# Kernel tuning notes

Hardware: AMD Instinct MI355X
Metric: run time of the kernel (lower is better)

The kernel has to match this reference:

```python
import jax, jax.numpy as jnp
import numpy as np

B, D_IN, UNITS, D_OUT = 16384, 1024, 512, 512
T_END = 0.1  # ODE integrated over t in (0, 0.1)


def setup_inputs() -> dict:
    key = jax.random.key(0)
    ks = jax.random.split(key, 8)
    return {
        "x": jax.random.normal(ks[0], (B, D_IN), dtype=jnp.float32),
        "w_in": jax.random.normal(ks[1], (UNITS, D_IN), dtype=jnp.float32) * 0.02,
        "b_in": jax.random.normal(ks[2], (UNITS,), dtype=jnp.float32) * 0.02,
        "sensory_w": jax.random.normal(ks[3], (UNITS, UNITS), dtype=jnp.float32) * 0.1,
        "sensory_sigma": jax.random.normal(ks[4], (UNITS,), dtype=jnp.float32) * 0.1,
        # tau = rand(units)*0.5 + 0.5  (in [0.5, 1.0])
        "tau": jax.random.uniform(ks[5], (UNITS,), dtype=jnp.float32) * 0.5 + 0.5,
        "readout_w": jax.random.normal(ks[6], (D_OUT, UNITS), dtype=jnp.float32) * 0.02,
        "readout_b": jax.random.normal(ks[7], (D_OUT,), dtype=jnp.float32) * 0.02,
        # liquid_state buffer starts at zeros, expanded to batch
        "states": jnp.zeros((B, UNITS), dtype=jnp.float32),
    }


def reference(x, w_in, b_in, sensory_w, sensory_sigma, tau, readout_w, readout_b, states):
    # input projection: tanh(Linear(x))
    projected = jnp.tanh(x @ w_in.T + b_in)                       # [B, U]
    # sensory activation A = sigmoid(projected @ sensory_w + sigma)
    A = jax.nn.sigmoid(projected @ sensory_w + sensory_sigma)     # [B, U]
    # ODE dy/dt = (-y + A)/tau has the closed-form solution
    #   y(t) = A + (y0 - A) * exp(-t / tau)
    # which is exactly what solve_ivp(RK45) approximates at t=0.1.
    decay = jnp.exp(-T_END / tau)                                 # [U]
    new_states = A + (states - A) * decay                         # [B, U]
    # readout
    output = new_states @ readout_w.T + readout_b                 # [B, D_OUT]
    return (output, new_states)
```

## Files before the change

kernel.cpp:

```cpp
#include <hip/hip_runtime.h>
#include <stdint.h>
#include <math.h>

typedef __bf16 bf16;
typedef __bf16 bf16x8 __attribute__((ext_vector_type(8)));
typedef __bf16 bf16x4 __attribute__((ext_vector_type(4)));
typedef float f32x4 __attribute__((ext_vector_type(4)));

static constexpr int BATCH = 16384;
static constexpr int D_IN  = 1024;
static constexpr int UNITS = 512;
static constexpr int D_OUT = 512;

__device__ __forceinline__ void gll16(const void* g, void* l) {
    __builtin_amdgcn_global_load_lds(
        (const __attribute__((address_space(1))) void*)g,
        (__attribute__((address_space(3))) void*)l,
        16, 0, 0);
}

template<int N>
__device__ __forceinline__ void waitvm() {
    static_assert(N < 16, "vmcnt imm");
    __builtin_amdgcn_s_waitcnt(0x0F70 | N);
    asm volatile("" ::: "memory");
}
__device__ __forceinline__ void barrier_raw() {
    asm volatile("" ::: "memory");
    __builtin_amdgcn_s_barrier();
    asm volatile("" ::: "memory");
}

__global__ __launch_bounds__(256)
void k_prep(const float* __restrict__ w_in, const float* __restrict__ sens_w,
            const float* __restrict__ ro_w,
            bf16* __restrict__ w_in_bf, bf16* __restrict__ sensT, bf16* __restrict__ ro_bf)
{
    __shared__ float tile[32][33];
    const int b = blockIdx.x;
    const int t = threadIdx.x;
    if (b < 512) {
        int i = b * 256 + t;
        f32x4 v = ((const f32x4*)w_in)[i];
        bf16x4 o = { (bf16)v.x, (bf16)v.y, (bf16)v.z, (bf16)v.w };
        ((bf16x4*)w_in_bf)[i] = o;
    } else if (b < 768) {
        int bb = b - 512;
        int bx = bb & 15, by = bb >> 4;
        int tx = t & 31, ty = t >> 5;
        #pragma unroll
        for (int j = ty; j < 32; j += 8)
            tile[j][tx] = sens_w[(size_t)(by * 32 + j) * UNITS + bx * 32 + tx];
        __syncthreads();
        #pragma unroll
        for (int j = ty; j < 32; j += 8)
            sensT[(size_t)(bx * 32 + j) * UNITS + by * 32 + tx] = (bf16)tile[tx][j];
    } else {
        int i = (b - 768) * 256 + t;
        f32x4 v = ((const f32x4*)ro_w)[i];
        bf16x4 o = { (bf16)v.x, (bf16)v.y, (bf16)v.z, (bf16)v.w };
        ((bf16x4*)ro_bf)[i] = o;
    }
}

template<int K, int EPI, bool AF32>
__global__ __launch_bounds__(512, 4)
void k_gemm(const float* __restrict__ Af, const bf16* __restrict__ Ab,
            const bf16* __restrict__ Bw,
            const float* __restrict__ bias,
            const float* __restrict__ tau,
            const float* __restrict__ states,
            float* __restrict__ outF, bf16* __restrict__ outB,
            int M, int N)
{
    constexpr int NSTEP = K / 32;
    constexpr int L = AF32 ? 3 : 2;
    constexpr int ABPB = AF32 ? (128 * 32 * 4) : (128 * 32 * 2);
    __shared__ __align__(16) char sAraw[3][ABPB];
    __shared__ bf16 sB[3][128 * 32];

    const int t = threadIdx.x;
    const int ntiles = N >> 7;
    const int nwg = gridDim.x;
    const int d = blockIdx.x;
    const int bid = (d & 7) * (nwg >> 3) + (d >> 3);
    const int mtile = bid / ntiles;
    const int ntile = bid % ntiles;
    const int m0 = mtile << 7, n0 = ntile << 7;

    const int lane = t & 63;
    const int wave = t >> 6;
    const int wr = (wave >> 1) * 32;
    const int wc = (wave & 1) * 64;
    const int l15 = lane & 15;
    const int lk  = (lane >> 4) * 8;

    f32x4 acc[2][4];
    #pragma unroll
    for (int m = 0; m < 2; ++m)
        #pragma unroll
        for (int n = 0; n < 4; ++n)
            acc[m][n] = (f32x4){0.f, 0.f, 0.f, 0.f};

    const int brow = t >> 2;
    const int bslot8 = ((t & 3) ^ ((brow >> 1) & 3)) * 8;
    const bf16* bbp = Bw + (size_t)(n0 + brow) * K + bslot8;
    const bf16* abp = AF32 ? nullptr : (Ab + (size_t)(m0 + brow) * K + bslot8);
    const int ar = t >> 3;
    const int aslot16 = ((t & 7) ^ (ar & 7)) * 16;
    const char* ag0 = (const char*)Af + (size_t)(m0 + ar) * K * 4 + aslot16;
    const char* ag1 = (const char*)Af + (size_t)(m0 + 64 + ar) * K * 4 + aslot16;

    auto STAGE = [&](int buf, int kt) {
        if constexpr (AF32) {
            gll16(ag0 + (size_t)kt * 4, &sAraw[buf][t * 16]);
            gll16(ag1 + (size_t)kt * 4, &sAraw[buf][8192 + t * 16]);
        } else {
            gll16(abp + kt, &sAraw[buf][t * 16]);
        }
        gll16(bbp + kt, (char*)&sB[buf][0] + t * 16);
    };

    int offB[4];
    #pragma unroll
    for (int n = 0; n < 4; ++n) {
        const int R = wc + n * 16 + l15;
        offB[n] = R * 64 + ((lk * 2) ^ (((R >> 1) & 3) << 4));
    }
    int offA0[2], offA1[2];
    #pragma unroll
    for (int m = 0; m < 2; ++m) {
        const int R = wr + m * 16 + l15;
        if constexpr (AF32) {
            const int s = (R & 7) << 4;
            offA0[m] = R * 128 + ((lk * 4) ^ s);
            offA1[m] = R * 128 + ((lk * 4 + 16) ^ s);
        } else {
            offA0[m] = R * 64 + ((lk * 2) ^ (((R >> 1) & 3) << 4));
        }
    }

    auto COMPUTE = [&](int buf) {
        const char* aB = &sAraw[buf][0];
        const char* bB = (const char*)&sB[buf][0];
        bf16x8 afr[2], bfr[4];
        if constexpr (AF32) {
            #pragma unroll
            for (int m = 0; m < 2; ++m) {
                f32x4 h0 = *(const f32x4*)(aB + offA0[m]);
                f32x4 h1 = *(const f32x4*)(aB + offA1[m]);
                afr[m] = (bf16x8){ (bf16)h0.x, (bf16)h0.y, (bf16)h0.z, (bf16)h0.w,
                                   (bf16)h1.x, (bf16)h1.y, (bf16)h1.z, (bf16)h1.w };
            }
        } else {
            #pragma unroll
            for (int m = 0; m < 2; ++m)
                afr[m] = *(const bf16x8*)(aB + offA0[m]);
        }
        #pragma unroll
        for (int n = 0; n < 4; ++n)
            bfr[n] = *(const bf16x8*)(bB + offB[n]);
        #pragma unroll
        for (int m = 0; m < 2; ++m)
            #pragma unroll
            for (int n = 0; n < 4; ++n)
                acc[m][n] = __builtin_amdgcn_mfma_f32_16x16x32_bf16(
                                afr[m], bfr[n], acc[m][n], 0, 0, 0);
    };

    STAGE(0, 0);
    STAGE(1, 32);
    STAGE(2, 64);

    int buf = 0;
    int kt_stage = 96;
    for (int i = 0; i < NSTEP - 2; ++i) {
        waitvm<2 * L>();
        barrier_raw();
        COMPUTE(buf);
        barrier_raw();
        if (kt_stage < K) { STAGE(buf, kt_stage); kt_stage += 32; }
        buf = (buf == 2) ? 0 : buf + 1;
    }
    waitvm<L>();
    barrier_raw();
    COMPUTE(buf);
    buf = (buf == 2) ? 0 : buf + 1;
    waitvm<0>();
    barrier_raw();
    COMPUTE(buf);
    asm volatile("" ::: "memory");

    const int rbase = m0 + wr + ((lane >> 4) << 2);
    const int cbase = n0 + wc + l15;
    #pragma unroll
    for (int n = 0; n < 4; ++n) {
        const int gc = cbase + n * 16;
        const float bv = bias[gc];
        float dec = 0.f;
        if constexpr (EPI == 2) dec = __expf(-0.1f / tau[gc]);
        #pragma unroll
        for (int m = 0; m < 2; ++m) {
            #pragma unroll
            for (int r = 0; r < 4; ++r) {
                const int gr = rbase + m * 16 + r;
                float v = acc[m][n][r] + bv;
                if constexpr (EPI == 1) {
                    float tv = 1.0f - 2.0f / (1.0f + __expf(2.0f * v));
                    outB[(size_t)gr * N + gc] = (bf16)tv;
                } else if constexpr (EPI == 2) {
                    float a = 1.0f / (1.0f + __expf(-v));
                    float s = states[(size_t)gr * N + gc];
                    outF[(size_t)gr * N + gc] = a + (s - a) * dec;
                } else {
                    outF[(size_t)gr * N + gc] = v;
                }
            }
        }
    }
}

extern "C" void kernel_launch(void* const* d_in, const int* in_sizes, int n_in,
                              void* d_out, int out_size, void* d_ws, size_t ws_size,
                              hipStream_t stream) {
    const float* x        = (const float*)d_in[0];
    const float* w_in     = (const float*)d_in[1];
    const float* b_in     = (const float*)d_in[2];
    const float* sens_w   = (const float*)d_in[3];
    const float* sens_sig = (const float*)d_in[4];
    const float* tau      = (const float*)d_in[5];
    const float* ro_w     = (const float*)d_in[6];
    const float* ro_b     = (const float*)d_in[7];
    const float* states   = (const float*)d_in[8];

    float* out    = (float*)d_out;
    float* new_st = out + (size_t)BATCH * D_OUT;
    bf16*  proj   = (bf16*)d_out;

    bf16* w_in_bf = (bf16*)d_ws;
    bf16* sensT   = w_in_bf + (size_t)UNITS * D_IN;
    bf16* ro_bf   = sensT + (size_t)UNITS * UNITS;

    k_prep<<<1024, 256, 0, stream>>>(w_in, sens_w, ro_w, w_in_bf, sensT, ro_bf);

    k_gemm<1024, 1, true><<<(BATCH / 128) * (UNITS / 128), 512, 0, stream>>>(
        x, nullptr, w_in_bf, b_in, nullptr, nullptr, nullptr, proj, BATCH, UNITS);

    k_gemm<512, 2, false><<<(BATCH / 128) * (UNITS / 128), 512, 0, stream>>>(
        nullptr, proj, sensT, sens_sig, tau, states, new_st, nullptr, BATCH, UNITS);

    k_gemm<512, 3, true><<<(BATCH / 128) * (D_OUT / 128), 512, 0, stream>>>(
        new_st, nullptr, ro_bf, ro_b, nullptr, nullptr, out, nullptr, BATCH, D_OUT);
}
```

Measured before the change: 79.64 us.

## Use 256-thread GEMM blocks with 64x64 warp tiles and per-GEMM pipeline depth

Changes the GEMM kernel from 8 waves computing 32x64 sub-tiles to 4 waves each computing 64x64 sub-tiles (4x4 MFMA accumulators), doubling fragment reuse per LDS read. The staging loads are redistributed so each thread issues more global-to-LDS copies, and the pipeline depth becomes a template parameter (2 stages for the fp32-input GEMMs, 3 for the bf16 one) to keep LDS usage bounded. This trades higher register pressure and fewer waves per block for less LDS traffic per MFMA, and the shallower prefetch may expose more memory latency.

```diff
diff --git a/kernel.cpp b/kernel.cpp
--- a/kernel.cpp
+++ b/kernel.cpp
@@ -63,8 +63,8 @@
     }
 }
 
-template<int K, int EPI, bool AF32>
-__global__ __launch_bounds__(512, 4)
+template<int K, int EPI, bool AF32, int DEPTH>
+__global__ __launch_bounds__(256, 2)
 void k_gemm(const float* __restrict__ Af, const bf16* __restrict__ Ab,
             const bf16* __restrict__ Bw,
             const float* __restrict__ bias,
@@ -74,10 +74,10 @@
             int M, int N)
 {
     constexpr int NSTEP = K / 32;
-    constexpr int L = AF32 ? 3 : 2;
-    constexpr int ABPB = AF32 ? (128 * 32 * 4) : (128 * 32 * 2);
-    __shared__ __align__(16) char sAraw[3][ABPB];
-    __shared__ bf16 sB[3][128 * 32];
+    constexpr int L = AF32 ? 6 : 4;
+    constexpr int ABPB = AF32 ? 16384 : 8192;
+    __shared__ __align__(16) char sAraw[DEPTH][ABPB];
+    __shared__ __align__(16) char sBraw[DEPTH][8192];
 
     const int t = threadIdx.x;
     const int ntiles = N >> 7;
@@ -90,105 +90,101 @@
 
     const int lane = t & 63;
     const int wave = t >> 6;
-    const int wr = (wave >> 1) * 32;
+    const int wr = (wave >> 1) * 64;
     const int wc = (wave & 1) * 64;
     const int l15 = lane & 15;
     const int lk  = (lane >> 4) * 8;
 
-    f32x4 acc[2][4];
+    f32x4 acc[4][4];
     #pragma unroll
-    for (int m = 0; m < 2; ++m)
+    for (int m = 0; m < 4; ++m)
         #pragma unroll
         for (int n = 0; n < 4; ++n)
             acc[m][n] = (f32x4){0.f, 0.f, 0.f, 0.f};
 
     const int brow = t >> 2;
-    const int bslot8 = ((t & 3) ^ ((brow >> 1) & 3)) * 8;
-    const bf16* bbp = Bw + (size_t)(n0 + brow) * K + bslot8;
-    const bf16* abp = AF32 ? nullptr : (Ab + (size_t)(m0 + brow) * K + bslot8);
+    const int bslot = ((t & 3) ^ ((brow >> 1) & 3)) * 16;
+    const char* bsrc = (const char*)Bw + (size_t)(n0 + brow) * K * 2 + bslot;
+    const char* asrcb = AF32 ? nullptr
+                             : ((const char*)Ab + (size_t)(m0 + brow) * K * 2 + bslot);
     const int ar = t >> 3;
-    const int aslot16 = ((t & 7) ^ (ar & 7)) * 16;
-    const char* ag0 = (const char*)Af + (size_t)(m0 + ar) * K * 4 + aslot16;
-    const char* ag1 = (const char*)Af + (size_t)(m0 + 64 + ar) * K * 4 + aslot16;
+    const int aslot = ((t & 7) ^ (ar & 7)) * 16;
+    const char* asrcf = AF32 ? ((const char*)Af + (size_t)(m0 + ar) * K * 4 + aslot)
+                             : nullptr;
 
     auto STAGE = [&](int buf, int kt) {
         if constexpr (AF32) {
-            gll16(ag0 + (size_t)kt * 4, &sAraw[buf][t * 16]);
-            gll16(ag1 + (size_t)kt * 4, &sAraw[buf][8192 + t * 16]);
+            const size_t kb = (size_t)kt * 4;
+            gll16(asrcf + kb,                      &sAraw[buf][t * 16]);
+            gll16(asrcf + kb + (size_t)32 * K * 4, &sAraw[buf][4096  + t * 16]);
+            gll16(asrcf + kb + (size_t)64 * K * 4, &sAraw[buf][8192  + t * 16]);
+            gll16(asrcf + kb + (size_t)96 * K * 4, &sAraw[buf][12288 + t * 16]);
         } else {
-            gll16(abp + kt, &sAraw[buf][t * 16]);
+            const size_t kb = (size_t)kt * 2;
+            gll16(asrcb + kb,                      &sAraw[buf][t * 16]);
+            gll16(asrcb + kb + (size_t)64 * K * 2, &sAraw[buf][4096 + t * 16]);
         }
-        gll16(bbp + kt, (char*)&sB[buf][0] + t * 16);
+        const size_t kb = (size_t)kt * 2;
+        gll16(bsrc + kb,                      &sBraw[buf][t * 16]);
+        gll16(bsrc + kb + (size_t)64 * K * 2, &sBraw[buf][4096 + t * 16]);
     };
 
-    int offB[4];
-    #pragma unroll
-    for (int n = 0; n < 4; ++n) {
-        const int R = wc + n * 16 + l15;
-        offB[n] = R * 64 + ((lk * 2) ^ (((R >> 1) & 3) << 4));
-    }
-    int offA0[2], offA1[2];
-    #pragma unroll
-    for (int m = 0; m < 2; ++m) {
-        const int R = wr + m * 16 + l15;
-        if constexpr (AF32) {
-            const int s = (R & 7) << 4;
-            offA0[m] = R * 128 + ((lk * 4) ^ s);
-            offA1[m] = R * 128 + ((lk * 4 + 16) ^ s);
-        } else {
-            offA0[m] = R * 64 + ((lk * 2) ^ (((R >> 1) & 3) << 4));
-        }
+    const int Rb = wc + l15;
+    const int boff = Rb * 64 + ((lk * 2) ^ (((Rb >> 1) & 3) << 4));
+    const int Ra = wr + l15;
+    int aoff0, aoff1 = 0;
+    if constexpr (AF32) {
+        const int s = (Ra & 7) << 4;
+        aoff0 = Ra * 128 + ((lk * 4) ^ s);
+        aoff1 = Ra * 128 + ((lk * 4 + 16) ^ s);
+    } else {
+        aoff0 = Ra * 64 + ((lk * 2) ^ (((Ra >> 1) & 3) << 4));
     }
 
     auto COMPUTE = [&](int buf) {
-        const char* aB = &sAraw[buf][0];
-        const char* bB = (const char*)&sB[buf][0];
-        bf16x8 afr[2], bfr[4];
-        if constexpr (AF32) {
-            #pragma unroll
-            for (int m = 0; m < 2; ++m) {
-                f32x4 h0 = *(const f32x4*)(aB + offA0[m]);
-                f32x4 h1 = *(const f32x4*)(aB + offA1[m]);
+        const char* aB = sAraw[buf];
+        const char* bB = sBraw[buf];
+        bf16x8 afr[4], bfr[4];
+        #pragma unroll
+        for (int m = 0; m < 4; ++m) {
+            if constexpr (AF32) {
+                f32x4 h0 = *(const f32x4*)(aB + aoff0 + m * 2048);
+                f32x4 h1 = *(const f32x4*)(aB + aoff1 + m * 2048);
                 afr[m] = (bf16x8){ (bf16)h0.x, (bf16)h0.y, (bf16)h0.z, (bf16)h0.w,
                                    (bf16)h1.x, (bf16)h1.y, (bf16)h1.z, (bf16)h1.w };
+            } else {
+                afr[m] = *(const bf16x8*)(aB + aoff0 + m * 1024);
             }
-        } else {
-            #pragma unroll
-            for (int m = 0; m < 2; ++m)
-                afr[m] = *(const bf16x8*)(aB + offA0[m]);
         }
         #pragma unroll
         for (int n = 0; n < 4; ++n)
-            bfr[n] = *(const bf16x8*)(bB + offB[n]);
-        #pragma unroll
-        for (int m = 0; m < 2; ++m)
+            bfr[n] = *(const bf16x8*)(bB + boff + n * 1024);
+        #pragma unroll
+        for (int m = 0; m < 4; ++m)
             #pragma unroll
             for (int n = 0; n < 4; ++n)
                 acc[m][n] = __builtin_amdgcn_mfma_f32_16x16x32_bf16(
                                 afr[m], bfr[n], acc[m][n], 0, 0, 0);
     };
 
-    STAGE(0, 0);
-    STAGE(1, 32);
-    STAGE(2, 64);
+    #pragma unroll
+    for (int p = 0; p < DEPTH; ++p) STAGE(p, p * 32);
 
     int buf = 0;
-    int kt_stage = 96;
-    for (int i = 0; i < NSTEP - 2; ++i) {
-        waitvm<2 * L>();
+    int kt_stage = DEPTH * 32;
+    for (int i = 0; i < NSTEP - (DEPTH - 1); ++i) {
+        waitvm<(DEPTH - 1) * L>();
         barrier_raw();
         COMPUTE(buf);
         barrier_raw();
         if (kt_stage < K) { STAGE(buf, kt_stage); kt_stage += 32; }
-        buf = (buf == 2) ? 0 : buf + 1;
-    }
-    waitvm<L>();
-    barrier_raw();
-    COMPUTE(buf);
-    buf = (buf == 2) ? 0 : buf + 1;
-    waitvm<0>();
-    barrier_raw();
-    COMPUTE(buf);
+        buf = (buf + 1 == DEPTH) ? 0 : buf + 1;
+    }
+    if constexpr (DEPTH == 3) {
+        waitvm<L>(); barrier_raw(); COMPUTE(buf);
+        buf = (buf + 1 == DEPTH) ? 0 : buf + 1;
+    }
+    waitvm<0>(); barrier_raw(); COMPUTE(buf);
     asm volatile("" ::: "memory");
 
     const int rbase = m0 + wr + ((lane >> 4) << 2);
@@ -200,7 +196,7 @@
         float dec = 0.f;
         if constexpr (EPI == 2) dec = __expf(-0.1f / tau[gc]);
         #pragma unroll
-        for (int m = 0; m < 2; ++m) {
+        for (int m = 0; m < 4; ++m) {
             #pragma unroll
             for (int r = 0; r < 4; ++r) {
                 const int gr = rbase + m * 16 + r;
@@ -243,12 +239,12 @@
 
     k_prep<<<1024, 256, 0, stream>>>(w_in, sens_w, ro_w, w_in_bf, sensT, ro_bf);
 
-    k_gemm<1024, 1, true><<<(BATCH / 128) * (UNITS / 128), 512, 0, stream>>>(
+    k_gemm<1024, 1, true, 2><<<(BATCH / 128) * (UNITS / 128), 256, 0, stream>>>(
         x, nullptr, w_in_bf, b_in, nullptr, nullptr, nullptr, proj, BATCH, UNITS);
 
-    k_gemm<512, 2, false><<<(BATCH / 128) * (UNITS / 128), 512, 0, stream>>>(
+    k_gemm<512, 2, false, 3><<<(BATCH / 128) * (UNITS / 128), 256, 0, stream>>>(
         nullptr, proj, sensT, sens_sig, tau, states, new_st, nullptr, BATCH, UNITS);
 
-    k_gemm<512, 3, true><<<(BATCH / 128) * (D_OUT / 128), 512, 0, stream>>>(
+    k_gemm<512, 3, true, 2><<<(BATCH / 128) * (D_OUT / 128), 256, 0, stream>>>(
         new_st, nullptr, ro_bf, ro_b, nullptr, nullptr, out, nullptr, BATCH, D_OUT);
 }
```

Result: no change. 81.15 us (+1.9%).

## Pre-pack x to swizzled bf16 tiles for the input projection GEMM

Applied to the files above, without the earlier changes.

Adds a pack pass that converts x from fp32 to bf16 and writes it in a per-tile, pre-swizzled contiguous layout stored temporarily in the new_states output region. The first GEMM then loads A with one contiguous 16-byte global-to-LDS load per step instead of two strided fp32 loads plus in-kernel conversion. This reduces LDS footprint and conversion work in the GEMM but adds an extra full read of x and a write and read of the packed copy.

```diff
diff --git a/kernel.cpp b/kernel.cpp
--- a/kernel.cpp
+++ b/kernel.cpp
@@ -32,20 +32,35 @@
 }
 
 __global__ __launch_bounds__(256)
-void k_prep(const float* __restrict__ w_in, const float* __restrict__ sens_w,
+void k_pack(const float* __restrict__ x, char* __restrict__ xp,
+            const float* __restrict__ w_in, const float* __restrict__ sens_w,
             const float* __restrict__ ro_w,
             bf16* __restrict__ w_in_bf, bf16* __restrict__ sensT, bf16* __restrict__ ro_bf)
 {
     __shared__ float tile[32][33];
     const int b = blockIdx.x;
     const int t = threadIdx.x;
-    if (b < 512) {
-        int i = b * 256 + t;
+    if (b < 4096) {
+        const int mt = b >> 5, j = b & 31;
+        #pragma unroll
+        for (int h = 0; h < 2; ++h) {
+            const int v = t + h * 256;
+            const int row = mt * 128 + (v >> 2);
+            const int kb = j * 32 + ((v & 3) ^ ((v >> 3) & 3)) * 8;
+            const float* src = x + (size_t)row * D_IN + kb;
+            f32x4 a = ((const f32x4*)src)[0];
+            f32x4 c = ((const f32x4*)src)[1];
+            bf16x8 o = { (bf16)a.x, (bf16)a.y, (bf16)a.z, (bf16)a.w,
+                         (bf16)c.x, (bf16)c.y, (bf16)c.z, (bf16)c.w };
+            *(bf16x8*)(xp + (size_t)b * 8192 + (size_t)v * 16) = o;
+        }
+    } else if (b < 4608) {
+        int i = (b - 4096) * 256 + t;
         f32x4 v = ((const f32x4*)w_in)[i];
         bf16x4 o = { (bf16)v.x, (bf16)v.y, (bf16)v.z, (bf16)v.w };
         ((bf16x4*)w_in_bf)[i] = o;
-    } else if (b < 768) {
-        int bb = b - 512;
+    } else if (b < 4864) {
+        int bb = b - 4608;
         int bx = bb & 15, by = bb >> 4;
         int tx = t & 31, ty = t >> 5;
         #pragma unroll
@@ -56,14 +71,14 @@
         for (int j = ty; j < 32; j += 8)
             sensT[(size_t)(bx * 32 + j) * UNITS + by * 32 + tx] = (bf16)tile[tx][j];
     } else {
-        int i = (b - 768) * 256 + t;
+        int i = (b - 4864) * 256 + t;
         f32x4 v = ((const f32x4*)ro_w)[i];
         bf16x4 o = { (bf16)v.x, (bf16)v.y, (bf16)v.z, (bf16)v.w };
         ((bf16x4*)ro_bf)[i] = o;
     }
 }
 
-template<int K, int EPI, bool AF32>
+template<int K, int EPI, bool AF32, bool APACK>
 __global__ __launch_bounds__(512, 4)
 void k_gemm(const float* __restrict__ Af, const bf16* __restrict__ Ab,
             const bf16* __restrict__ Bw,
@@ -105,7 +120,9 @@
     const int brow = t >> 2;
     const int bslot8 = ((t & 3) ^ ((brow >> 1) & 3)) * 8;
     const bf16* bbp = Bw + (size_t)(n0 + brow) * K + bslot8;
-    const bf16* abp = AF32 ? nullptr : (Ab + (size_t)(m0 + brow) * K + bslot8);
+    const bf16* abp = (AF32 || APACK) ? nullptr : (Ab + (size_t)(m0 + brow) * K + bslot8);
+    const char* apk = APACK ? ((const char*)Ab + (size_t)mtile * NSTEP * 8192 + (size_t)t * 16)
+                            : nullptr;
     const int ar = t >> 3;
     const int aslot16 = ((t & 7) ^ (ar & 7)) * 16;
     const char* ag0 = (const char*)Af + (size_t)(m0 + ar) * K * 4 + aslot16;
@@ -115,6 +132,8 @@
         if constexpr (AF32) {
             gll16(ag0 + (size_t)kt * 4, &sAraw[buf][t * 16]);
             gll16(ag1 + (size_t)kt * 4, &sAraw[buf][8192 + t * 16]);
+        } else if constexpr (APACK) {
+            gll16(apk + (size_t)kt * 256, &sAraw[buf][t * 16]);
         } else {
             gll16(abp + kt, &sAraw[buf][t * 16]);
         }
@@ -236,19 +255,19 @@
     float* out    = (float*)d_out;
     float* new_st = out + (size_t)BATCH * D_OUT;
     bf16*  proj   = (bf16*)d_out;
-
+    char*  xp     = (char*)new_st;
     bf16* w_in_bf = (bf16*)d_ws;
     bf16* sensT   = w_in_bf + (size_t)UNITS * D_IN;
     bf16* ro_bf   = sensT + (size_t)UNITS * UNITS;
 
-    k_prep<<<1024, 256, 0, stream>>>(w_in, sens_w, ro_w, w_in_bf, sensT, ro_bf);
-
-    k_gemm<1024, 1, true><<<(BATCH / 128) * (UNITS / 128), 512, 0, stream>>>(
-        x, nullptr, w_in_bf, b_in, nullptr, nullptr, nullptr, proj, BATCH, UNITS);
-
-    k_gemm<512, 2, false><<<(BATCH / 128) * (UNITS / 128), 512, 0, stream>>>(
+    k_pack<<<5120, 256, 0, stream>>>(x, xp, w_in, sens_w, ro_w, w_in_bf, sensT, ro_bf);
+
+    k_gemm<1024, 1, false, true><<<(BATCH / 128) * (UNITS / 128), 512, 0, stream>>>(
+        nullptr, (const bf16*)xp, w_in_bf, b_in, nullptr, nullptr, nullptr, proj, BATCH, UNITS);
+
+    k_gemm<512, 2, false, false><<<(BATCH / 128) * (UNITS / 128), 512, 0, stream>>>(
         nullptr, proj, sensT, sens_sig, tau, states, new_st, nullptr, BATCH, UNITS);
 
-    k_gemm<512, 3, true><<<(BATCH / 128) * (D_OUT / 128), 512, 0, stream>>>(
+    k_gemm<512, 3, true, false><<<(BATCH / 128) * (D_OUT / 128), 512, 0, stream>>>(
         new_st, nullptr, ro_bf, ro_b, nullptr, nullptr, out, nullptr, BATCH, D_OUT);
 }
```

New measurement: 85.54 us. 7.4% more time.

## Fuse three GEMMs into one kernel keeping row-block activations in LDS

Applied to the files above, without the earlier changes.

Replaces the three separate GEMM launches with one fused kernel. Each workgroup owns 64 batch rows across the full 512-wide unit dimension and keeps the tanh projection and the new states as bf16 in swizzled LDS between stages. This removes the global round-trips of the bf16 projection and the readback of new_states, plus two launches. In exchange it uses 144KB of LDS per block, only 256 workgroups and double rather than triple buffering, and every block restreams full weight matrices, which lowers occupancy and raises weight traffic.

```diff
diff --git a/kernel.cpp b/kernel.cpp
--- a/kernel.cpp
+++ b/kernel.cpp
@@ -63,160 +63,228 @@
     }
 }
 
-template<int K, int EPI, bool AF32>
-__global__ __launch_bounds__(512, 4)
-void k_gemm(const float* __restrict__ Af, const bf16* __restrict__ Ab,
-            const bf16* __restrict__ Bw,
-            const float* __restrict__ bias,
-            const float* __restrict__ tau,
-            const float* __restrict__ states,
-            float* __restrict__ outF, bf16* __restrict__ outB,
-            int M, int N)
+__global__ __launch_bounds__(512, 2)
+void k_fused(const float* __restrict__ x,
+             const bf16* __restrict__ w_in_bf, const float* __restrict__ b_in,
+             const bf16* __restrict__ sensT,   const float* __restrict__ sens_sig,
+             const bf16* __restrict__ ro_bf,   const float* __restrict__ ro_b,
+             const float* __restrict__ tau,    const float* __restrict__ states,
+             float* __restrict__ out, float* __restrict__ new_st)
 {
-    constexpr int NSTEP = K / 32;
-    constexpr int L = AF32 ? 3 : 2;
-    constexpr int ABPB = AF32 ? (128 * 32 * 4) : (128 * 32 * 2);
-    __shared__ __align__(16) char sAraw[3][ABPB];
-    __shared__ bf16 sB[3][128 * 32];
+    extern __shared__ __align__(16) char smem[];
+    char* sA = smem;
+    char* sB = smem + 16384;
+    char* sP = smem + 81920;
 
     const int t = threadIdx.x;
-    const int ntiles = N >> 7;
-    const int nwg = gridDim.x;
     const int d = blockIdx.x;
-    const int bid = (d & 7) * (nwg >> 3) + (d >> 3);
-    const int mtile = bid / ntiles;
-    const int ntile = bid % ntiles;
-    const int m0 = mtile << 7, n0 = ntile << 7;
+    const int bid = (d & 7) * 32 + (d >> 3);
+    const int m0 = bid << 6;
 
     const int lane = t & 63;
     const int wave = t >> 6;
-    const int wr = (wave >> 1) * 32;
-    const int wc = (wave & 1) * 64;
-    const int l15 = lane & 15;
-    const int lk  = (lane >> 4) * 8;
-
-    f32x4 acc[2][4];
-    #pragma unroll
-    for (int m = 0; m < 2; ++m)
-        #pragma unroll
-        for (int n = 0; n < 4; ++n)
-            acc[m][n] = (f32x4){0.f, 0.f, 0.f, 0.f};
-
-    const int brow = t >> 2;
-    const int bslot8 = ((t & 3) ^ ((brow >> 1) & 3)) * 8;
-    const bf16* bbp = Bw + (size_t)(n0 + brow) * K + bslot8;
-    const bf16* abp = AF32 ? nullptr : (Ab + (size_t)(m0 + brow) * K + bslot8);
-    const int ar = t >> 3;
-    const int aslot16 = ((t & 7) ^ (ar & 7)) * 16;
-    const char* ag0 = (const char*)Af + (size_t)(m0 + ar) * K * 4 + aslot16;
-    const char* ag1 = (const char*)Af + (size_t)(m0 + 64 + ar) * K * 4 + aslot16;
-
-    auto STAGE = [&](int buf, int kt) {
-        if constexpr (AF32) {
-            gll16(ag0 + (size_t)kt * 4, &sAraw[buf][t * 16]);
-            gll16(ag1 + (size_t)kt * 4, &sAraw[buf][8192 + t * 16]);
-        } else {
-            gll16(abp + kt, &sAraw[buf][t * 16]);
-        }
-        gll16(bbp + kt, (char*)&sB[buf][0] + t * 16);
+    const int wc   = wave << 6;
+    const int l15  = lane & 15;
+    const int lk   = (lane >> 4) << 3;
+    const int r0   = (lane >> 4) << 2;
+
+    const int brow  = t >> 2;
+    const int bslot = ((t & 3) ^ ((brow >> 1) & 3)) << 4;
+    const int ar    = t >> 3;
+    const int aslot = ((t & 7) ^ (ar & 7)) << 4;
+    const char* xsrc = (const char*)x + (size_t)(m0 + ar) * (D_IN * 4) + aslot;
+
+    int boff[4];
+    #pragma unroll
+    for (int n = 0; n < 4; ++n) {
+        const int R = wc + n * 16 + l15;
+        boff[n] = R * 64 + ((lk * 2) ^ (((R >> 1) & 3) << 4));
+    }
+    int aoff0[4], aoff1[4], prow[4], pswz[4];
+    #pragma unroll
+    for (int m = 0; m < 4; ++m) {
+        const int R = m * 16 + l15;
+        const int s = (R & 7) << 4;
+        aoff0[m] = R * 128 + ((lk * 4) ^ s);
+        aoff1[m] = R * 128 + ((lk * 4 + 16) ^ s);
+        prow[m]  = R * 1024;
+        pswz[m]  = R & 7;
+    }
+    const int pslotk = lk >> 3;
+
+    f32x4 acc[4][4];
+
+    auto zacc = [&]() {
+        #pragma unroll
+        for (int m = 0; m < 4; ++m)
+            #pragma unroll
+            for (int n = 0; n < 4; ++n)
+                acc[m][n] = (f32x4){0.f, 0.f, 0.f, 0.f};
     };
-
-    int offB[4];
-    #pragma unroll
-    for (int n = 0; n < 4; ++n) {
-        const int R = wc + n * 16 + l15;
-        offB[n] = R * 64 + ((lk * 2) ^ (((R >> 1) & 3) << 4));
-    }
-    int offA0[2], offA1[2];
-    #pragma unroll
-    for (int m = 0; m < 2; ++m) {
-        const int R = wr + m * 16 + l15;
-        if constexpr (AF32) {
-            const int s = (R & 7) << 4;
-            offA0[m] = R * 128 + ((lk * 4) ^ s);
-            offA1[m] = R * 128 + ((lk * 4 + 16) ^ s);
-        } else {
-            offA0[m] = R * 64 + ((lk * 2) ^ (((R >> 1) & 3) << 4));
-        }
-    }
-
-    auto COMPUTE = [&](int buf) {
-        const char* aB = &sAraw[buf][0];
-        const char* bB = (const char*)&sB[buf][0];
-        bf16x8 afr[2], bfr[4];
-        if constexpr (AF32) {
-            #pragma unroll
-            for (int m = 0; m < 2; ++m) {
-                f32x4 h0 = *(const f32x4*)(aB + offA0[m]);
-                f32x4 h1 = *(const f32x4*)(aB + offA1[m]);
+    auto stageB = [&](int buf, const char* Bb, int kbytes, int kt) {
+        const size_t ko = (size_t)kt * 2 + bslot;
+        #pragma unroll
+        for (int j = 0; j < 4; ++j)
+            gll16(Bb + (size_t)(j * 128 + brow) * kbytes + ko,
+                  sB + (buf << 15) + (j << 13) + (t << 4));
+    };
+    auto stageA = [&](int buf, int kt) {
+        gll16(xsrc + (size_t)kt * 4, sA + (buf << 13) + (t << 4));
+    };
+
+    zacc();
+    {
+        const char* Bb = (const char*)w_in_bf;
+        stageA(0, 0);
+        stageB(0, Bb, D_IN * 2, 0);
+        for (int i = 0; i < 32; ++i) {
+            const int cur = i & 1;
+            if (i < 31) {
+                stageA(cur ^ 1, (i + 1) * 32);
+                stageB(cur ^ 1, Bb, D_IN * 2, (i + 1) * 32);
+                waitvm<5>();
+            } else {
+                waitvm<0>();
+            }
+            barrier_raw();
+            const char* aB = sA + (cur << 13);
+            const char* bB = sB + (cur << 15);
+            bf16x8 afr[4], bfr[4];
+            #pragma unroll
+            for (int m = 0; m < 4; ++m) {
+                f32x4 h0 = *(const f32x4*)(aB + aoff0[m]);
+                f32x4 h1 = *(const f32x4*)(aB + aoff1[m]);
                 afr[m] = (bf16x8){ (bf16)h0.x, (bf16)h0.y, (bf16)h0.z, (bf16)h0.w,
                                    (bf16)h1.x, (bf16)h1.y, (bf16)h1.z, (bf16)h1.w };
             }
-        } else {
-            #pragma unroll
-            for (int m = 0; m < 2; ++m)
-                afr[m] = *(const bf16x8*)(aB + offA0[m]);
+            #pragma unroll
+            for (int n = 0; n < 4; ++n)
+                bfr[n] = *(const bf16x8*)(bB + boff[n]);
+            #pragma unroll
+            for (int m = 0; m < 4; ++m)
+                #pragma unroll
+                for (int n = 0; n < 4; ++n)
+                    acc[m][n] = __builtin_amdgcn_mfma_f32_16x16x32_bf16(
+                                    afr[m], bfr[n], acc[m][n], 0, 0, 0);
+            barrier_raw();
         }
-        #pragma unroll
-        for (int n = 0; n < 4; ++n)
-            bfr[n] = *(const bf16x8*)(bB + offB[n]);
-        #pragma unroll
-        for (int m = 0; m < 2; ++m)
+    }
+    #pragma unroll
+    for (int n = 0; n < 4; ++n) {
+        const int gc = wc + n * 16 + l15;
+        const float bv = b_in[gc];
+        #pragma unroll
+        for (int m = 0; m < 4; ++m)
+            #pragma unroll
+            for (int r = 0; r < 4; ++r) {
+                const int grow = m * 16 + r0 + r;
+                float v = acc[m][n][r] + bv;
+                float tv = 1.0f - 2.0f / (1.0f + __expf(2.0f * v));
+                *(bf16*)(sP + grow * 1024 +
+                         ((((gc >> 3) ^ (grow & 7)) << 4) | ((gc & 7) << 1))) = (bf16)tv;
+            }
+    }
+    __syncthreads();
+
+    zacc();
+    {
+        const char* Bb = (const char*)sensT;
+        stageB(0, Bb, UNITS * 2, 0);
+        for (int i = 0; i < 16; ++i) {
+            const int cur = i & 1;
+            if (i < 15) { stageB(cur ^ 1, Bb, UNITS * 2, (i + 1) * 32); waitvm<4>(); }
+            else        { waitvm<0>(); }
+            barrier_raw();
+            const char* bB = sB + (cur << 15);
+            bf16x8 afr[4], bfr[4];
+            #pragma unroll
+            for (int m = 0; m < 4; ++m)
+                afr[m] = *(const bf16x8*)(sP + prow[m] +
+                            ((((i << 2) + pslotk) ^ pswz[m]) << 4));
             #pragma unroll
             for (int n = 0; n < 4; ++n)
-                acc[m][n] = __builtin_amdgcn_mfma_f32_16x16x32_bf16(
-                                afr[m], bfr[n], acc[m][n], 0, 0, 0);
-    };
-
-    STAGE(0, 0);
-    STAGE(1, 32);
-    STAGE(2, 64);
-
-    int buf = 0;
-    int kt_stage = 96;
-    for (int i = 0; i < NSTEP - 2; ++i) {
-        waitvm<2 * L>();
-        barrier_raw();
-        COMPUTE(buf);
-        barrier_raw();
-        if (kt_stage < K) { STAGE(buf, kt_stage); kt_stage += 32; }
-        buf = (buf == 2) ? 0 : buf + 1;
-    }
-    waitvm<L>();
-    barrier_raw();
-    COMPUTE(buf);
-    buf = (buf == 2) ? 0 : buf + 1;
-    waitvm<0>();
-    barrier_raw();
-    COMPUTE(buf);
-    asm volatile("" ::: "memory");
-
-    const int rbase = m0 + wr + ((lane >> 4) << 2);
-    const int cbase = n0 + wc + l15;
-    #pragma unroll
-    for (int n = 0; n < 4; ++n) {
-        const int gc = cbase + n * 16;
-        const float bv = bias[gc];
-        float dec = 0.f;
-        if constexpr (EPI == 2) dec = __expf(-0.1f / tau[gc]);
-        #pragma unroll
-        for (int m = 0; m < 2; ++m) {
+                bfr[n] = *(const bf16x8*)(bB + boff[n]);
+            #pragma unroll
+            for (int m = 0; m < 4; ++m)
+                #pragma unroll
+                for (int n = 0; n < 4; ++n)
+                    acc[m][n] = __builtin_amdgcn_mfma_f32_16x16x32_bf16(
+                                    afr[m], bfr[n], acc[m][n], 0, 0, 0);
+            barrier_raw();
+        }
+    }
+    #pragma unroll
+    for (int n = 0; n < 4; ++n) {
+        const int gc = wc + n * 16 + l15;
+        const float sg  = sens_sig[gc];
+        const float dec = __expf(-0.1f / tau[gc]);
+        #pragma unroll
+        for (int m = 0; m < 4; ++m)
             #pragma unroll
             for (int r = 0; r < 4; ++r) {
-                const int gr = rbase + m * 16 + r;
-                float v = acc[m][n][r] + bv;
-                if constexpr (EPI == 1) {
-                    float tv = 1.0f - 2.0f / (1.0f + __expf(2.0f * v));
-                    outB[(size_t)gr * N + gc] = (bf16)tv;
-                } else if constexpr (EPI == 2) {
-                    float a = 1.0f / (1.0f + __expf(-v));
-                    float s = states[(size_t)gr * N + gc];
-                    outF[(size_t)gr * N + gc] = a + (s - a) * dec;
-                } else {
-                    outF[(size_t)gr * N + gc] = v;
-                }
-            }
+                const int grow = m * 16 + r0 + r;
+                float v = acc[m][n][r] + sg;
+                float a = 1.0f / (1.0f + __expf(-v));
+                float s = states[(size_t)(m0 + grow) * UNITS + gc];
+                float ns = a + (s - a) * dec;
+                new_st[(size_t)(m0 + grow) * UNITS + gc] = ns;
+                acc[m][n][r] = ns;
+            }
+    }
+    __syncthreads();
+    #pragma unroll
+    for (int n = 0; n < 4; ++n) {
+        const int gc = wc + n * 16 + l15;
+        #pragma unroll
+        for (int m = 0; m < 4; ++m)
+            #pragma unroll
+            for (int r = 0; r < 4; ++r) {
+                const int grow = m * 16 + r0 + r;
+                *(bf16*)(sP + grow * 1024 +
+                         ((((gc >> 3) ^ (grow & 7)) << 4) | ((gc & 7) << 1)))
+                    = (bf16)acc[m][n][r];
+            }
+    }
+    __syncthreads();
+
+    zacc();
+    {
+        const char* Bb = (const char*)ro_bf;
+        stageB(0, Bb, UNITS * 2, 0);
+        for (int i = 0; i < 16; ++i) {
+            const int cur = i & 1;
+            if (i < 15) { stageB(cur ^ 1, Bb, UNITS * 2, (i + 1) * 32); waitvm<4>(); }
+            else        { waitvm<0>(); }
+            barrier_raw();
+            const char* bB = sB + (cur << 15);
+            bf16x8 afr[4], bfr[4];
+            #pragma unroll
+            for (int m = 0; m < 4; ++m)
+                afr[m] = *(const bf16x8*)(sP + prow[m] +
+                            ((((i << 2) + pslotk) ^ pswz[m]) << 4));
+            #pragma unroll
+            for (int n = 0; n < 4; ++n)
+                bfr[n] = *(const bf16x8*)(bB + boff[n]);
+            #pragma unroll
+            for (int m = 0; m < 4; ++m)
+                #pragma unroll
+                for (int n = 0; n < 4; ++n)
+                    acc[m][n] = __builtin_amdgcn_mfma_f32_16x16x32_bf16(
+                                    afr[m], bfr[n], acc[m][n], 0, 0, 0);
+            barrier_raw();
         }
+    }
+    #pragma unroll
+    for (int n = 0; n < 4; ++n) {
+        const int gc = wc + n * 16 + l15;
+        const float rb = ro_b[gc];
+        #pragma unroll
+        for (int m = 0; m < 4; ++m)
+            #pragma unroll
+            for (int r = 0; r < 4; ++r) {
+                const int grow = m * 16 + r0 + r;
+                out[(size_t)(m0 + grow) * D_OUT + gc] = acc[m][n][r] + rb;
+            }
     }
 }
 
@@ -235,7 +303,6 @@
 
     float* out    = (float*)d_out;
     float* new_st = out + (size_t)BATCH * D_OUT;
-    bf16*  proj   = (bf16*)d_out;
 
     bf16* w_in_bf = (bf16*)d_ws;
     bf16* sensT   = w_in_bf + (size_t)UNITS * D_IN;
@@ -243,12 +310,9 @@
 
     k_prep<<<1024, 256, 0, stream>>>(w_in, sens_w, ro_w, w_in_bf, sensT, ro_bf);
 
-    k_gemm<1024, 1, true><<<(BATCH / 128) * (UNITS / 128), 512, 0, stream>>>(
-        x, nullptr, w_in_bf, b_in, nullptr, nullptr, nullptr, proj, BATCH, UNITS);
-
-    k_gemm<512, 2, false><<<(BATCH / 128) * (UNITS / 128), 512, 0, stream>>>(
-        nullptr, proj, sensT, sens_sig, tau, states, new_st, nullptr, BATCH, UNITS);
-
-    k_gemm<512, 3, true><<<(BATCH / 128) * (D_OUT / 128), 512, 0, stream>>>(
-        new_st, nullptr, ro_bf, ro_b, nullptr, nullptr, out, nullptr, BATCH, D_OUT);
-}
+    constexpr int SMEM = 16384 + 65536 + 65536;
+    (void)hipFuncSetAttribute(reinterpret_cast<const void*>(&k_fused),
+                              hipFuncAttributeMaxDynamicSharedMemorySize, SMEM);
+    k_fused<<<BATCH / 64, 512, SMEM, stream>>>(
+        x, w_in_bf, b_in, sensT, sens_sig, ro_bf, ro_b, tau, states, out, new_st);
+}
```

Result: slower. 117.4 us (+47.4%).
